# Kernel optimization log

Hardware: AMD Instinct MI355X
Metric: run time of the kernel (lower is better)

## Reference

```python
import jax, jax.numpy as jnp
import numpy as np

B, N, DIM = 8, 256, 256
INTER = DIM // 4          # downsample=4
POS_H = 64                # pos_mlp_hidden_dim
ATTN_H = INTER * 4        # attn_mlp_hidden_mult=4


def setup_inputs() -> dict:
    key = jax.random.key(0)
    ks = jax.random.split(key, 16)
    s = lambda fan_in: 1.0 / np.sqrt(fan_in)
    return {
        "x": jax.random.normal(ks[0], (B, N, DIM), jnp.float32),
        "y": jax.random.normal(ks[1], (B, N, DIM), jnp.float32),
        "x_pos": jax.random.normal(ks[2], (B, N, 3), jnp.float32),
        "y_pos": jax.random.normal(ks[3], (B, N, 3), jnp.float32),
        "mask": jax.random.randint(ks[4], (B, N), 0, 2) > 0,
        # linear weights stored (in, out) for direct matmul; torch Linear has no bias for g/theta/phi/conv_out
        "g_w": jax.random.normal(ks[5], (DIM, INTER), jnp.float32) * s(DIM),
        "theta_w": jax.random.normal(ks[6], (DIM, INTER), jnp.float32) * s(DIM),
        "phi_w": jax.random.normal(ks[7], (DIM, INTER), jnp.float32) * s(DIM),
        "pos_w1": jax.random.normal(ks[8], (3, POS_H), jnp.float32) * s(3),
        "pos_b1": jnp.zeros((POS_H,), jnp.float32),
        "pos_w2": jax.random.normal(ks[9], (POS_H, INTER), jnp.float32) * s(POS_H),
        "pos_b2": jnp.zeros((INTER,), jnp.float32),
        "attn_w1": jax.random.normal(ks[10], (INTER, ATTN_H), jnp.float32) * s(INTER),
        "attn_b1": jnp.zeros((ATTN_H,), jnp.float32),
        "attn_w2": jax.random.normal(ks[11], (ATTN_H, INTER), jnp.float32) * s(ATTN_H),
        "attn_b2": jnp.zeros((INTER,), jnp.float32),
        "out_w": jax.random.normal(ks[12], (INTER, DIM), jnp.float32) * s(INTER),
    }


def reference(x, y, x_pos, y_pos, mask, g_w, theta_w, phi_w,
              pos_w1, pos_b1, pos_w2, pos_b2,
              attn_w1, attn_b1, attn_w2, attn_b2, out_w):
    v = y @ g_w            # (b, j, d)
    q = x @ theta_w        # (b, i, d)
    k = y @ phi_w          # (b, j, d)
    # pairwise relative positions -> MLP embedding, (b, i, j, d)
    rel_pos = x_pos[:, :, None, :] - y_pos[:, None, :, :]
    rel_pos_emb = jax.nn.relu(rel_pos @ pos_w1 + pos_b1) @ pos_w2 + pos_b2
    # MLP-based attention score on (q_i - k_j + rel_pos_emb)
    qk_rel = q[:, :, None, :] - k[:, None, :, :]
    sim = jax.nn.relu((qk_rel + rel_pos_emb) @ attn_w1 + attn_b1) @ attn_w2 + attn_b2
    # masked softmax over j (dim=-2)
    pair_mask = mask[:, :, None] & mask[:, None, :]      # (b, i, j)
    neg = -jnp.finfo(sim.dtype).max
    sim = jnp.where(pair_mask[..., None], sim, neg)
    attn = jax.nn.softmax(sim, axis=-2)
    # value + positional embedding, then per-channel weighted aggregate over j
    v_full = v[:, None, :, :] + rel_pos_emb              # (b, i, j, d)
    agg = jnp.einsum('bijd,bijd->bid', attn, v_full)
    return x + agg @ out_w
```

## Files before the change

kernel.cpp:

```cpp
#include <hip/hip_runtime.h>
#include <hip/hip_bf16.h>

#define NB 8
#define NN 256
#define DIMV 256
#define DI 64
#define NEGMAX 3.402823466e+38f

typedef unsigned short u16;
typedef unsigned int u32;
typedef __attribute__((ext_vector_type(8))) short bf16x8;
typedef __attribute__((ext_vector_type(4))) float f32x4;
typedef __attribute__((ext_vector_type(2))) float f32x2;
typedef __attribute__((ext_vector_type(2))) unsigned int u32x2;

__device__ __forceinline__ u16 f2bf(float f) {
    __hip_bfloat16 h = __float2bfloat16(f);
    u16 u; __builtin_memcpy(&u, &h, 2); return u;
}
__device__ __forceinline__ u32 pack2(float a, float b) {
    return (u32)f2bf(a) | ((u32)f2bf(b) << 16);
}
__device__ __forceinline__ float ubf_lo(u32 u) {
    union { u32 u; float f; } x; x.u = u << 16; return x.f;
}
__device__ __forceinline__ float ubf_hi(u32 u) {
    union { u32 u; float f; } x; x.u = u & 0xffff0000u; return x.f;
}
__device__ __forceinline__ int fA(int row) { return ((row & 7) << 4) ^ ((row & 8) << 2); }
__device__ __forceinline__ int fB(int row) { return ((row >> 1) & 7) << 4; }

__global__ void prep_w(const float* __restrict__ w1, const float* __restrict__ w2,
                       const float* __restrict__ pw2,
                       u16* __restrict__ w1s, u16* __restrict__ w2s, u16* __restrict__ pw2s)
{
    const int idx = blockIdx.x * 256 + threadIdx.x;
    const int e   = idx & 7;
    const int l   = (idx >> 3) & 63;
    const int l15 = l & 15, lh = l >> 4;
    {
        const int frag = idx >> 9;
        const int ks = frag & 1, c2 = (frag >> 1) & 1, hc = frag >> 2;
        w1s[idx] = f2bf(w1[(ks * 32 + lh * 8 + e) * 256 + hc * 32 + 2 * l15 + c2]);
    }
    {
        const int frag = idx >> 9;
        const int ct = frag & 3, hc = frag >> 2;
        w2s[idx] = f2bf(w2[(hc * 32 + lh * 8 + e) * 64 + 4 * l15 + ct]);
    }
    if (idx < 4096) {
        const int frag = idx >> 9;
        const int ks = frag & 1, ct = frag >> 1;
        pw2s[idx] = f2bf(pw2[(ks * 32 + lh * 8 + e) * 64 + 4 * l15 + ct]);
    }
}

__global__ void prep_qkv(const float* __restrict__ x, const float* __restrict__ y,
                         const float* __restrict__ tw, const float* __restrict__ pw,
                         const float* __restrict__ gw,
                         float* __restrict__ q, float* __restrict__ k, float* __restrict__ v)
{
    __shared__ float xs[4][256];
    __shared__ float ys[4][256];
    const int blk = blockIdx.x;
    const int b = blk >> 6;
    const int n0 = (blk & 63) * 4;
    const int tid = threadIdx.x;
    {
        int r = tid >> 6, e = tid & 63;
        ((float4*)xs[r])[e] = ((const float4*)(x + (size_t)(b * NN + n0 + r) * DIMV))[e];
        ((float4*)ys[r])[e] = ((const float4*)(y + (size_t)(b * NN + n0 + r) * DIMV))[e];
    }
    __syncthreads();
    const int nl = tid >> 6, d = tid & 63;
    float aq = 0.f, ak = 0.f, av = 0.f;
    #pragma unroll 4
    for (int c = 0; c < 256; ++c) {
        float wq = tw[c * 64 + d], wk = pw[c * 64 + d], wv = gw[c * 64 + d];
        float xv = xs[nl][c], yv = ys[nl][c];
        aq += xv * wq; ak += yv * wk; av += yv * wv;
    }
    const int n = n0 + nl;
    q[(b * NN + n) * DI + d] = aq;
    k[(b * NN + n) * DI + d] = ak;
    v[(b * NN + n) * DI + d] = av;
}

__global__ __launch_bounds__(256, 2)
void fused_attn(const float* __restrict__ x, const float* __restrict__ x_pos,
                const float* __restrict__ y_pos, const int* __restrict__ mask,
                const float* __restrict__ pw1, const float* __restrict__ pb1,
                const float* __restrict__ pb2,
                const float* __restrict__ ab1, const float* __restrict__ ab2,
                const float* __restrict__ out_w,
                const float* __restrict__ qg, const float* __restrict__ kg,
                const float* __restrict__ vg,
                const u16* __restrict__ w1s, const u16* __restrict__ w2s,
                const u16* __restrict__ pw2s,
                float* __restrict__ out)
{
    __shared__ __align__(16) char sStg[4][4096];
    __shared__ __align__(16) char sV2[4][4096];

    const int blk = blockIdx.x;
    const int b = blk >> 8;
    const int i = blk & 255;
    const int tid = threadIdx.x;
    const int l   = tid & 63;
    const int w   = tid >> 6;
    const int j0  = w * 64;
    const int l15 = l & 15;
    const int lh  = l >> 4;

    char* const stg  = sStg[w];
    char* const sV2w = sV2[w];
    float* const sRedF = (float*)&sStg[0][0];

    int stW[4], hcW[4];
    #pragma unroll
    for (int r = 0; r < 4; ++r) {
        const int lr = lh * 4 + r;
        stW[r] = (lr * 128 + l15 * 8) ^ fA(lr);
        hcW[r] = (lr * 64 + l15 * 4) ^ fB(lr);
    }
    const int stR0 = (l15 * 128 + lh * 16) ^ fA(l15);
    const int stR1 = stR0 ^ 64;
    const int hcR  = (l15 * 64 + lh * 16) ^ fB(l15);

    const int mjl = mask[b * NN + j0 + l];
    const unsigned long long mb = __ballot(mjl != 0);
    const bool mi_b = mask[b * NN + i] != 0;

    const float xp0 = x_pos[(b * NN + i) * 3 + 0];
    const float xp1 = x_pos[(b * NN + i) * 3 + 1];
    const float xp2 = x_pos[(b * NN + i) * 3 + 2];

    bf16x8 af[4][2];
    {
        float rel[4][3];
        #pragma unroll
        for (int rt = 0; rt < 4; ++rt) {
            const float* yp = y_pos + (size_t)(b * NN + j0 + rt * 16 + l15) * 3;
            rel[rt][0] = xp0 - yp[0];
            rel[rt][1] = xp1 - yp[1];
            rel[rt][2] = xp2 - yp[2];
        }
        #pragma unroll
        for (int ks = 0; ks < 2; ++ks) {
            const int c0 = ks * 32 + lh * 8;
            float w0[8], w1c[8], w2c[8], bb[8];
            #pragma unroll
            for (int qq = 0; qq < 2; ++qq) {
                *(f32x4*)&w0[qq*4]  = *(const f32x4*)&pw1[0*64 + c0 + qq*4];
                *(f32x4*)&w1c[qq*4] = *(const f32x4*)&pw1[1*64 + c0 + qq*4];
                *(f32x4*)&w2c[qq*4] = *(const f32x4*)&pw1[2*64 + c0 + qq*4];
                *(f32x4*)&bb[qq*4]  = *(const f32x4*)&pb1[c0 + qq*4];
            }
            #pragma unroll
            for (int rt = 0; rt < 4; ++rt) {
                bf16x8 v;
                #pragma unroll
                for (int cc = 0; cc < 8; ++cc) {
                    float h = bb[cc] + rel[rt][0]*w0[cc] + rel[rt][1]*w1c[cc] + rel[rt][2]*w2c[cc];
                    v[cc] = (short)f2bf(fmaxf(h, 0.f));
                }
                af[rt][ks] = v;
            }
        }
    }

    const f32x4 qv   = *(const f32x4*)&qg[((size_t)b * NN + i) * DI + 4 * l15];
    const f32x4 pb2v = *(const f32x4*)&pb2[4 * l15];
    bf16x8 bfr[4][2];
    #pragma unroll
    for (int ct = 0; ct < 4; ++ct)
        #pragma unroll
        for (int ks = 0; ks < 2; ++ks)
            bfr[ct][ks] = *(const bf16x8*)(pw2s + ((ct * 2 + ks) * 64 + l) * 8);

    bf16x8 aT[4][2];
    u32x2 accVp[2][4];
    #pragma unroll
    for (int rt = 0; rt < 4; ++rt) {
        f32x4 accR[4];
        #pragma unroll
        for (int ct = 0; ct < 4; ++ct) {
            f32x4 a = {pb2v[ct], pb2v[ct], pb2v[ct], pb2v[ct]};
            a = __builtin_amdgcn_mfma_f32_16x16x32_bf16(af[rt][0], bfr[ct][0], a, 0, 0, 0);
            a = __builtin_amdgcn_mfma_f32_16x16x32_bf16(af[rt][1], bfr[ct][1], a, 0, 0, 0);
            accR[ct] = a;
        }
        #pragma unroll
        for (int r = 0; r < 4; ++r) {
            const int row = j0 + rt * 16 + lh * 4 + r;
            const f32x4 kv = *(const f32x4*)&kg[((size_t)b * NN + row) * DI + 4 * l15];
            const f32x4 vv = *(const f32x4*)&vg[((size_t)b * NN + row) * DI + 4 * l15];
            float tv[4], vf[4];
            #pragma unroll
            for (int ct = 0; ct < 4; ++ct) {
                const float rpe = accR[ct][r];
                tv[ct] = qv[ct] - kv[ct] + rpe;
                vf[ct] = vv[ct] + rpe;
            }
            u32x2 tpk; tpk[0] = pack2(tv[0], tv[1]); tpk[1] = pack2(tv[2], tv[3]);
            u32x2 vpk; vpk[0] = pack2(vf[0], vf[1]); vpk[1] = pack2(vf[2], vf[3]);
            *(u32x2*)(stg + stW[r]) = tpk;
            if (rt < 2) accVp[rt][r] = vpk;
            else        *(u32x2*)(sV2w + stW[r] + (rt - 2) * 2048) = vpk;
        }
        aT[rt][0] = *(const bf16x8*)(stg + stR0);
        aT[rt][1] = *(const bf16x8*)(stg + stR1);
    }

    const f32x4 ab2v = *(const f32x4*)&ab2[4 * l15];
    f32x4 accS[4][4];
    #pragma unroll
    for (int rt = 0; rt < 4; ++rt)
        #pragma unroll
        for (int ct = 0; ct < 4; ++ct)
            accS[rt][ct] = (f32x4){ab2v[ct], ab2v[ct], ab2v[ct], ab2v[ct]};

    #pragma unroll 2
    for (int hc = 0; hc < 8; ++hc) {
        bf16x8 b1f[2][2];
        #pragma unroll
        for (int c2 = 0; c2 < 2; ++c2)
            #pragma unroll
            for (int ks = 0; ks < 2; ++ks)
                b1f[c2][ks] = *(const bf16x8*)(w1s + ((hc * 4 + c2 * 2 + ks) * 64 + l) * 8);
        bf16x8 b2f[4];
        #pragma unroll
        for (int ct = 0; ct < 4; ++ct)
            b2f[ct] = *(const bf16x8*)(w2s + ((hc * 4 + ct) * 64 + l) * 8);
        const f32x2 ab1v = *(const f32x2*)&ab1[hc * 32 + 2 * l15];
        const f32x4 ib0 = {ab1v[0], ab1v[0], ab1v[0], ab1v[0]};
        const f32x4 ib1 = {ab1v[1], ab1v[1], ab1v[1], ab1v[1]};
        #pragma unroll
        for (int rt = 0; rt < 4; ++rt) {
            f32x4 h0 = ib0, h1 = ib1;
            h0 = __builtin_amdgcn_mfma_f32_16x16x32_bf16(aT[rt][0], b1f[0][0], h0, 0, 0, 0);
            h0 = __builtin_amdgcn_mfma_f32_16x16x32_bf16(aT[rt][1], b1f[0][1], h0, 0, 0, 0);
            h1 = __builtin_amdgcn_mfma_f32_16x16x32_bf16(aT[rt][0], b1f[1][0], h1, 0, 0, 0);
            h1 = __builtin_amdgcn_mfma_f32_16x16x32_bf16(aT[rt][1], b1f[1][1], h1, 0, 0, 0);
            #pragma unroll
            for (int r = 0; r < 4; ++r)
                *(u32*)(stg + hcW[r] + rt * 1024) =
                    pack2(fmaxf(h0[r], 0.f), fmaxf(h1[r], 0.f));
        }
        #pragma unroll
        for (int rt = 0; rt < 4; ++rt) {
            bf16x8 a2 = *(const bf16x8*)(stg + hcR + rt * 1024);
            #pragma unroll
            for (int ct = 0; ct < 4; ++ct)
                accS[rt][ct] = __builtin_amdgcn_mfma_f32_16x16x32_bf16(a2, b2f[ct], accS[rt][ct], 0, 0, 0);
        }
    }

    float mx[4] = {-NEGMAX, -NEGMAX, -NEGMAX, -NEGMAX};
    #pragma unroll
    for (int rt = 0; rt < 4; ++rt)
        #pragma unroll
        for (int r = 0; r < 4; ++r) {
            const int ro = rt * 16 + lh * 4 + r;
            const bool bit = mi_b && ((mb >> ro) & 1ull);
            #pragma unroll
            for (int ct = 0; ct < 4; ++ct) {
                float s = bit ? accS[rt][ct][r] : -NEGMAX;
                accS[rt][ct][r] = s;
                mx[ct] = fmaxf(mx[ct], s);
            }
        }
    #pragma unroll
    for (int ct = 0; ct < 4; ++ct) {
        mx[ct] = fmaxf(mx[ct], __shfl_xor(mx[ct], 16));
        mx[ct] = fmaxf(mx[ct], __shfl_xor(mx[ct], 32));
    }
    __syncthreads();
    if (lh == 0)
        *(f32x4*)&sRedF[w * 64 + 4 * l15] = (f32x4){mx[0], mx[1], mx[2], mx[3]};
    __syncthreads();
    float m4[4];
    {
        f32x4 a0 = *(f32x4*)&sRedF[      4 * l15];
        f32x4 a1 = *(f32x4*)&sRedF[ 64 + 4 * l15];
        f32x4 a2 = *(f32x4*)&sRedF[128 + 4 * l15];
        f32x4 a3 = *(f32x4*)&sRedF[192 + 4 * l15];
        #pragma unroll
        for (int ct = 0; ct < 4; ++ct)
            m4[ct] = fmaxf(fmaxf(a0[ct], a1[ct]), fmaxf(a2[ct], a3[ct]));
    }
    float ssum[4] = {0.f, 0.f, 0.f, 0.f}, sagg[4] = {0.f, 0.f, 0.f, 0.f};
    #pragma unroll
    for (int rt = 0; rt < 4; ++rt)
        #pragma unroll
        for (int r = 0; r < 4; ++r) {
            u32x2 vpk;
            if (rt < 2) vpk = accVp[rt][r];
            else        vpk = *(const u32x2*)(sV2w + stW[r] + (rt - 2) * 2048);
            const float vfs[4] = {ubf_lo(vpk[0]), ubf_hi(vpk[0]), ubf_lo(vpk[1]), ubf_hi(vpk[1])};
            #pragma unroll
            for (int ct = 0; ct < 4; ++ct) {
                const float e = __expf(accS[rt][ct][r] - m4[ct]);
                ssum[ct] += e;
                sagg[ct] += e * vfs[ct];
            }
        }
    #pragma unroll
    for (int ct = 0; ct < 4; ++ct) {
        ssum[ct] += __shfl_xor(ssum[ct], 16);
        ssum[ct] += __shfl_xor(ssum[ct], 32);
        sagg[ct] += __shfl_xor(sagg[ct], 16);
        sagg[ct] += __shfl_xor(sagg[ct], 32);
    }
    if (lh == 0) {
        *(f32x4*)&sRedF[256 + w * 64 + 4 * l15] = (f32x4){ssum[0], ssum[1], ssum[2], ssum[3]};
        *(f32x4*)&sRedF[512 + w * 64 + 4 * l15] = (f32x4){sagg[0], sagg[1], sagg[2], sagg[3]};
    }
    __syncthreads();
    if (tid < 64) {
        float den = sRedF[256 + tid] + sRedF[320 + tid] + sRedF[384 + tid] + sRedF[448 + tid];
        float ag  = sRedF[512 + tid] + sRedF[576 + tid] + sRedF[640 + tid] + sRedF[704 + tid];
        sRedF[768 + tid] = ag / den;
    }
    __syncthreads();

    {
        float acc = 0.f;
        #pragma unroll 8
        for (int d = 0; d < 64; ++d)
            acc += sRedF[768 + d] * out_w[d * DIMV + tid];
        const int o = (b * NN + i) * DIMV + tid;
        out[o] = x[o] + acc;
    }
}

extern "C" void kernel_launch(void* const* d_in, const int* in_sizes, int n_in,
                              void* d_out, int out_size, void* d_ws, size_t ws_size,
                              hipStream_t stream)
{
    const float* x       = (const float*)d_in[0];
    const float* y       = (const float*)d_in[1];
    const float* x_pos   = (const float*)d_in[2];
    const float* y_pos   = (const float*)d_in[3];
    const int*   mask    = (const int*)d_in[4];
    const float* g_w     = (const float*)d_in[5];
    const float* theta_w = (const float*)d_in[6];
    const float* phi_w   = (const float*)d_in[7];
    const float* pos_w1  = (const float*)d_in[8];
    const float* pos_b1  = (const float*)d_in[9];
    const float* pos_w2  = (const float*)d_in[10];
    const float* pos_b2  = (const float*)d_in[11];
    const float* attn_w1 = (const float*)d_in[12];
    const float* attn_b1 = (const float*)d_in[13];
    const float* attn_w2 = (const float*)d_in[14];
    const float* attn_b2 = (const float*)d_in[15];
    const float* out_w   = (const float*)d_in[16];

    float* q = (float*)d_ws;
    float* k = q + NB * NN * DI;
    float* v = k + NB * NN * DI;
    u16* w1s  = (u16*)(v + NB * NN * DI);
    u16* w2s  = w1s + 16384;
    u16* pw2s = w2s + 16384;

    prep_w<<<64, 256, 0, stream>>>(attn_w1, attn_w2, pos_w2, w1s, w2s, pw2s);
    prep_qkv<<<512, 256, 0, stream>>>(x, y, theta_w, phi_w, g_w, q, k, v);
    fused_attn<<<NB * NN, 256, 0, stream>>>(x, x_pos, y_pos, mask,
                                            pos_w1, pos_b1, pos_b2,
                                            attn_b1, attn_b2, out_w,
                                            q, k, v, w1s, w2s, pw2s,
                                            (float*)d_out);
}
```

Before: 93.58 us.

## Merge prep kernels, compute pos MLP layer1 via MFMA, add setprio and unroll

Merges the weight-swizzle and QKV projection kernels into one launch with 16 rows per block and vectorized float4 weight loads. The first positional-MLP layer (3->64 plus bias) is now done as a zero-padded bf16 MFMA against a pre-swizzled weight fragment and restaged through LDS, replacing per-lane scalar FMAs. It also raises wave priority around the attention-MLP MFMA section and unrolls the output projection loop further. The cost is extra LDS traffic and bf16 rounding of the relative positions, plus fewer prep blocks for the QKV work.

```diff
diff --git a/kernel.cpp b/kernel.cpp
--- a/kernel.cpp
+++ b/kernel.cpp
@@ -30,73 +30,92 @@
 __device__ __forceinline__ int fA(int row) { return ((row & 7) << 4) ^ ((row & 8) << 2); }
 __device__ __forceinline__ int fB(int row) { return ((row >> 1) & 7) << 4; }
 
-__global__ void prep_w(const float* __restrict__ w1, const float* __restrict__ w2,
-                       const float* __restrict__ pw2,
-                       u16* __restrict__ w1s, u16* __restrict__ w2s, u16* __restrict__ pw2s)
-{
-    const int idx = blockIdx.x * 256 + threadIdx.x;
-    const int e   = idx & 7;
-    const int l   = (idx >> 3) & 63;
-    const int l15 = l & 15, lh = l >> 4;
-    {
-        const int frag = idx >> 9;
-        const int ks = frag & 1, c2 = (frag >> 1) & 1, hc = frag >> 2;
-        w1s[idx] = f2bf(w1[(ks * 32 + lh * 8 + e) * 256 + hc * 32 + 2 * l15 + c2]);
-    }
-    {
-        const int frag = idx >> 9;
-        const int ct = frag & 3, hc = frag >> 2;
-        w2s[idx] = f2bf(w2[(hc * 32 + lh * 8 + e) * 64 + 4 * l15 + ct]);
-    }
-    if (idx < 4096) {
-        const int frag = idx >> 9;
-        const int ks = frag & 1, ct = frag >> 1;
-        pw2s[idx] = f2bf(pw2[(ks * 32 + lh * 8 + e) * 64 + 4 * l15 + ct]);
-    }
-}
-
-__global__ void prep_qkv(const float* __restrict__ x, const float* __restrict__ y,
+__global__ void prep_all(const float* __restrict__ x, const float* __restrict__ y,
                          const float* __restrict__ tw, const float* __restrict__ pw,
                          const float* __restrict__ gw,
-                         float* __restrict__ q, float* __restrict__ k, float* __restrict__ v)
+                         const float* __restrict__ w1, const float* __restrict__ w2,
+                         const float* __restrict__ pw2,
+                         const float* __restrict__ pw1, const float* __restrict__ pb1,
+                         float* __restrict__ q, float* __restrict__ k, float* __restrict__ v,
+                         u16* __restrict__ w1s, u16* __restrict__ w2s,
+                         u16* __restrict__ pw2s, u16* __restrict__ pw1f)
 {
-    __shared__ float xs[4][256];
-    __shared__ float ys[4][256];
+    __shared__ float xs[16][256];
+    __shared__ float ys[16][256];
     const int blk = blockIdx.x;
-    const int b = blk >> 6;
-    const int n0 = (blk & 63) * 4;
     const int tid = threadIdx.x;
+
+    if (blk >= 128) {
+        const int idx = (blk - 128) * 256 + tid;
+        const int e   = idx & 7;
+        const int l   = (idx >> 3) & 63;
+        const int l15 = l & 15, lh = l >> 4;
+        {
+            const int frag = idx >> 9;
+            const int ks = frag & 1, c2 = (frag >> 1) & 1, hc = frag >> 2;
+            w1s[idx] = f2bf(w1[(ks * 32 + lh * 8 + e) * 256 + hc * 32 + 2 * l15 + c2]);
+        }
+        {
+            const int frag = idx >> 9;
+            const int ct = frag & 3, hc = frag >> 2;
+            w2s[idx] = f2bf(w2[(hc * 32 + lh * 8 + e) * 64 + 4 * l15 + ct]);
+        }
+        if (idx < 4096) {
+            const int frag = idx >> 9;
+            const int ks = frag & 1, ct = frag >> 1;
+            pw2s[idx] = f2bf(pw2[(ks * 32 + lh * 8 + e) * 64 + 4 * l15 + ct]);
+        }
+        if (idx < 2048) {
+            const int ct = idx >> 9;
+            const int kk = lh * 8 + e;
+            const int col = 4 * l15 + ct;
+            float val = (kk < 3) ? pw1[kk * 64 + col] : ((kk == 3) ? pb1[col] : 0.f);
+            pw1f[idx] = f2bf(val);
+        }
+        return;
+    }
+
+    const int b = blk >> 4;
+    const int n0 = (blk & 15) * 16;
     {
-        int r = tid >> 6, e = tid & 63;
-        ((float4*)xs[r])[e] = ((const float4*)(x + (size_t)(b * NN + n0 + r) * DIMV))[e];
-        ((float4*)ys[r])[e] = ((const float4*)(y + (size_t)(b * NN + n0 + r) * DIMV))[e];
-    }
-    __syncthreads();
-    const int nl = tid >> 6, d = tid & 63;
-    float aq = 0.f, ak = 0.f, av = 0.f;
+        const f32x4* xsrc = (const f32x4*)(x + (size_t)(b * NN + n0) * DIMV);
+        const f32x4* ysrc = (const f32x4*)(y + (size_t)(b * NN + n0) * DIMV);
+        f32x4* xd = (f32x4*)&xs[0][0];
+        f32x4* yd = (f32x4*)&ys[0][0];
+        #pragma unroll
+        for (int qq = 0; qq < 4; ++qq) {
+            xd[qq * 256 + tid] = xsrc[qq * 256 + tid];
+            yd[qq * 256 + tid] = ysrc[qq * 256 + tid];
+        }
+    }
+    __syncthreads();
+    const int nl = tid >> 4;
+    const int d0 = (tid & 15) * 4;
+    f32x4 aq = {0.f,0.f,0.f,0.f}, ak = {0.f,0.f,0.f,0.f}, av = {0.f,0.f,0.f,0.f};
     #pragma unroll 4
     for (int c = 0; c < 256; ++c) {
-        float wq = tw[c * 64 + d], wk = pw[c * 64 + d], wv = gw[c * 64 + d];
-        float xv = xs[nl][c], yv = ys[nl][c];
+        const f32x4 wq = *(const f32x4*)&tw[c * 64 + d0];
+        const f32x4 wk = *(const f32x4*)&pw[c * 64 + d0];
+        const f32x4 wv = *(const f32x4*)&gw[c * 64 + d0];
+        const float xv = xs[nl][c], yv = ys[nl][c];
         aq += xv * wq; ak += yv * wk; av += yv * wv;
     }
     const int n = n0 + nl;
-    q[(b * NN + n) * DI + d] = aq;
-    k[(b * NN + n) * DI + d] = ak;
-    v[(b * NN + n) * DI + d] = av;
+    *(f32x4*)&q[((size_t)b * NN + n) * DI + d0] = aq;
+    *(f32x4*)&k[((size_t)b * NN + n) * DI + d0] = ak;
+    *(f32x4*)&v[((size_t)b * NN + n) * DI + d0] = av;
 }
 
 __global__ __launch_bounds__(256, 2)
 void fused_attn(const float* __restrict__ x, const float* __restrict__ x_pos,
                 const float* __restrict__ y_pos, const int* __restrict__ mask,
-                const float* __restrict__ pw1, const float* __restrict__ pb1,
                 const float* __restrict__ pb2,
                 const float* __restrict__ ab1, const float* __restrict__ ab2,
                 const float* __restrict__ out_w,
                 const float* __restrict__ qg, const float* __restrict__ kg,
                 const float* __restrict__ vg,
                 const u16* __restrict__ w1s, const u16* __restrict__ w2s,
-                const u16* __restrict__ pw2s,
+                const u16* __restrict__ pw2s, const u16* __restrict__ pw1f,
                 float* __restrict__ out)
 {
     __shared__ __align__(16) char sStg[4][4096];
@@ -113,6 +132,7 @@
     const int lh  = l >> 4;
 
     char* const stg  = sStg[w];
+    char* const stgB = sStg[w] + 2048;
     char* const sV2w = sV2[w];
     float* const sRedF = (float*)&sStg[0][0];
 
@@ -135,39 +155,21 @@
     const float xp1 = x_pos[(b * NN + i) * 3 + 1];
     const float xp2 = x_pos[(b * NN + i) * 3 + 2];
 
-    bf16x8 af[4][2];
-    {
-        float rel[4][3];
-        #pragma unroll
-        for (int rt = 0; rt < 4; ++rt) {
-            const float* yp = y_pos + (size_t)(b * NN + j0 + rt * 16 + l15) * 3;
-            rel[rt][0] = xp0 - yp[0];
-            rel[rt][1] = xp1 - yp[1];
-            rel[rt][2] = xp2 - yp[2];
-        }
-        #pragma unroll
-        for (int ks = 0; ks < 2; ++ks) {
-            const int c0 = ks * 32 + lh * 8;
-            float w0[8], w1c[8], w2c[8], bb[8];
-            #pragma unroll
-            for (int qq = 0; qq < 2; ++qq) {
-                *(f32x4*)&w0[qq*4]  = *(const f32x4*)&pw1[0*64 + c0 + qq*4];
-                *(f32x4*)&w1c[qq*4] = *(const f32x4*)&pw1[1*64 + c0 + qq*4];
-                *(f32x4*)&w2c[qq*4] = *(const f32x4*)&pw1[2*64 + c0 + qq*4];
-                *(f32x4*)&bb[qq*4]  = *(const f32x4*)&pb1[c0 + qq*4];
-            }
-            #pragma unroll
-            for (int rt = 0; rt < 4; ++rt) {
-                bf16x8 v;
-                #pragma unroll
-                for (int cc = 0; cc < 8; ++cc) {
-                    float h = bb[cc] + rel[rt][0]*w0[cc] + rel[rt][1]*w1c[cc] + rel[rt][2]*w2c[cc];
-                    v[cc] = (short)f2bf(fmaxf(h, 0.f));
-                }
-                af[rt][ks] = v;
-            }
-        }
-    }
+    bf16x8 afr[4];
+    #pragma unroll
+    for (int rt = 0; rt < 4; ++rt) {
+        const float* yp = y_pos + (size_t)(b * NN + j0 + rt * 16 + l15) * 3;
+        const float r0 = xp0 - yp[0], r1 = xp1 - yp[1], r2 = xp2 - yp[2];
+        union { u32 u[4]; bf16x8 v; } c;
+        c.u[0] = (lh == 0) ? pack2(r0, r1) : 0u;
+        c.u[1] = (lh == 0) ? pack2(r2, 1.0f) : 0u;
+        c.u[2] = 0u; c.u[3] = 0u;
+        afr[rt] = c.v;
+    }
+    bf16x8 pw1b[4];
+    #pragma unroll
+    for (int ct = 0; ct < 4; ++ct)
+        pw1b[ct] = *(const bf16x8*)(pw1f + (ct * 64 + l) * 8);
 
     const f32x4 qv   = *(const f32x4*)&qg[((size_t)b * NN + i) * DI + 4 * l15];
     const f32x4 pb2v = *(const f32x4*)&pb2[4 * l15];
@@ -182,12 +184,28 @@
     u32x2 accVp[2][4];
     #pragma unroll
     for (int rt = 0; rt < 4; ++rt) {
+        f32x4 hA[4];
+        #pragma unroll
+        for (int ct = 0; ct < 4; ++ct) {
+            f32x4 z = {0.f, 0.f, 0.f, 0.f};
+            hA[ct] = __builtin_amdgcn_mfma_f32_16x16x32_bf16(afr[rt], pw1b[ct], z, 0, 0, 0);
+        }
+        #pragma unroll
+        for (int r = 0; r < 4; ++r) {
+            u32x2 hpk;
+            hpk[0] = pack2(fmaxf(hA[0][r], 0.f), fmaxf(hA[1][r], 0.f));
+            hpk[1] = pack2(fmaxf(hA[2][r], 0.f), fmaxf(hA[3][r], 0.f));
+            *(u32x2*)(stgB + stW[r]) = hpk;
+        }
+        const bf16x8 afc0 = *(const bf16x8*)(stgB + stR0);
+        const bf16x8 afc1 = *(const bf16x8*)(stgB + stR1);
+
         f32x4 accR[4];
         #pragma unroll
         for (int ct = 0; ct < 4; ++ct) {
             f32x4 a = {pb2v[ct], pb2v[ct], pb2v[ct], pb2v[ct]};
-            a = __builtin_amdgcn_mfma_f32_16x16x32_bf16(af[rt][0], bfr[ct][0], a, 0, 0, 0);
-            a = __builtin_amdgcn_mfma_f32_16x16x32_bf16(af[rt][1], bfr[ct][1], a, 0, 0, 0);
+            a = __builtin_amdgcn_mfma_f32_16x16x32_bf16(afc0, bfr[ct][0], a, 0, 0, 0);
+            a = __builtin_amdgcn_mfma_f32_16x16x32_bf16(afc1, bfr[ct][1], a, 0, 0, 0);
             accR[ct] = a;
         }
         #pragma unroll
@@ -235,6 +253,7 @@
         const f32x2 ab1v = *(const f32x2*)&ab1[hc * 32 + 2 * l15];
         const f32x4 ib0 = {ab1v[0], ab1v[0], ab1v[0], ab1v[0]};
         const f32x4 ib1 = {ab1v[1], ab1v[1], ab1v[1], ab1v[1]};
+        __builtin_amdgcn_s_setprio(1);
         #pragma unroll
         for (int rt = 0; rt < 4; ++rt) {
             f32x4 h0 = ib0, h1 = ib1;
@@ -245,7 +264,7 @@
             #pragma unroll
             for (int r = 0; r < 4; ++r)
                 *(u32*)(stg + hcW[r] + rt * 1024) =
-                    pack2(fmaxf(h0[r], 0.f), fmaxf(h1[r], 0.f));
+                    pack2(fmaxf(h0[r] , 0.f), fmaxf(h1[r], 0.f));
         }
         #pragma unroll
         for (int rt = 0; rt < 4; ++rt) {
@@ -254,6 +273,7 @@
             for (int ct = 0; ct < 4; ++ct)
                 accS[rt][ct] = __builtin_amdgcn_mfma_f32_16x16x32_bf16(a2, b2f[ct], accS[rt][ct], 0, 0, 0);
         }
+        __builtin_amdgcn_s_setprio(0);
     }
 
     float mx[4] = {-NEGMAX, -NEGMAX, -NEGMAX, -NEGMAX};
@@ -326,7 +346,7 @@
 
     {
         float acc = 0.f;
-        #pragma unroll 8
+        #pragma unroll 16
         for (int d = 0; d < 64; ++d)
             acc += sRedF[768 + d] * out_w[d * DIMV + tid];
         const int o = (b * NN + i) * DIMV + tid;
@@ -362,12 +382,13 @@
     u16* w1s  = (u16*)(v + NB * NN * DI);
     u16* w2s  = w1s + 16384;
     u16* pw2s = w2s + 16384;
-
-    prep_w<<<64, 256, 0, stream>>>(attn_w1, attn_w2, pos_w2, w1s, w2s, pw2s);
-    prep_qkv<<<512, 256, 0, stream>>>(x, y, theta_w, phi_w, g_w, q, k, v);
+    u16* pw1f = pw2s + 4096;
+
+    prep_all<<<192, 256, 0, stream>>>(x, y, theta_w, phi_w, g_w,
+                                      attn_w1, attn_w2, pos_w2, pos_w1, pos_b1,
+                                      q, k, v, w1s, w2s, pw2s, pw1f);
     fused_attn<<<NB * NN, 256, 0, stream>>>(x, x_pos, y_pos, mask,
-                                            pos_w1, pos_b1, pos_b2,
-                                            attn_b1, attn_b2, out_w,
-                                            q, k, v, w1s, w2s, pw2s,
+                                            pos_b2, attn_b1, attn_b2, out_w,
+                                            q, k, v, w1s, w2s, pw2s, pw1f,
                                             (float*)d_out);
 }
```

New measurement: 94.08 us. Within noise of the previous version (+0.5%).
